# Kernel tuning notes

Measured on AMD Instinct MI355X. Metric: run time of the kernel, lower is better.

## Reference

```python
import jax, jax.numpy as jnp
import numpy as np

B, T, S, E, H, F = 4, 1024, 1024, 512, 8, 2048
D = E // H  # head_dim = 64
SCALE = D ** -0.5
EPS = 1e-5


def setup_inputs() -> dict:
    key = jax.random.key(0)
    ks = jax.random.split(key, 16)
    w = lambda k, shape: jax.random.normal(k, shape, jnp.float32) * 0.02
    inp = {
        'tgt': jax.random.normal(ks[0], (B, T, E), jnp.float32),
        'memory': jax.random.normal(ks[1], (B, S, E), jnp.float32),
    }
    for i, n in enumerate(['sWq', 'sWk', 'sWv', 'sWo', 'cWq', 'cWk', 'cWv', 'cWo']):
        inp[n] = w(ks[2 + i], (E, E))
    for n in ['sbq', 'sbk', 'sbv', 'sbo', 'cbq', 'cbk', 'cbv', 'cbo']:
        inp[n] = jnp.zeros((E,), jnp.float32)
    inp['fW1'] = w(ks[10], (E, F)); inp['fb1'] = jnp.zeros((F,), jnp.float32)
    inp['fW2'] = w(ks[11], (F, E)); inp['fb2'] = jnp.zeros((E,), jnp.float32)
    for n in ['g1', 'g2', 'g3']:
        inp[n] = jnp.ones((E,), jnp.float32)
    for n in ['be1', 'be2', 'be3']:
        inp[n] = jnp.zeros((E,), jnp.float32)
    return inp


def _ln(x, g, b):
    mu = jnp.mean(x, axis=-1, keepdims=True)
    var = jnp.mean(jnp.square(x - mu), axis=-1, keepdims=True)
    return (x - mu) * jax.lax.rsqrt(var + EPS) * g + b


def _mha(xq, xkv, Wq, bq, Wk, bk, Wv, bv, Wo, bo):
    # dense-equivalent of full N^2 edge-list attention (softmax over source nodes per target)
    Bq, Tq, _ = xq.shape
    Skv = xkv.shape[1]
    q = (xq @ Wq + bq).reshape(Bq, Tq, H, D)
    k = (xkv @ Wk + bk).reshape(Bq, Skv, H, D)
    v = (xkv @ Wv + bv).reshape(Bq, Skv, H, D)
    scores = jnp.einsum('bthd,bshd->bhts', q, k) * SCALE
    wts = jax.nn.softmax(scores, axis=-1)
    out = jnp.einsum('bhts,bshd->bthd', wts, v).reshape(Bq, Tq, E)
    return out @ Wo + bo


def reference(tgt, memory,
              sWq, sbq, sWk, sbk, sWv, sbv, sWo, sbo,
              cWq, cbq, cWk, cbk, cWv, cbv, cWo, cbo,
              fW1, fb1, fW2, fb2,
              g1, be1, g2, be2, g3, be3):
    # post-norm decoder layer: self-attn -> cross-attn -> FFN (dropout=0 eval)
    x = _ln(tgt + _mha(tgt, tgt, sWq, sbq, sWk, sbk, sWv, sbv, sWo, sbo), g1, be1)
    x = _ln(x + _mha(x, memory, cWq, cbq, cWk, cbk, cWv, cbv, cWo, cbo), g2, be2)
    ff = jax.nn.relu(x @ fW1 + fb1) @ fW2 + fb2
    x = _ln(x + ff, g3, be3)
    return x
```

## Files before the change

kernel.cpp:

```cpp
#include <hip/hip_runtime.h>

typedef unsigned short ushort_t;
typedef short short8 __attribute__((ext_vector_type(8)));
typedef float float4v __attribute__((ext_vector_type(4)));

__device__ __forceinline__ float bf2f(ushort_t u) {
    union { unsigned int i; float f; } x; x.i = ((unsigned int)u) << 16; return x.f;
}
__device__ __forceinline__ ushort_t f2bf(float f) {
    unsigned int u = __float_as_uint(f);
    unsigned int r = (u + 0x7FFFu + ((u >> 16) & 1u)) >> 16;
    return (ushort_t)r;
}
__device__ __forceinline__ void store_out(float* p, float v) { *p = v; }
__device__ __forceinline__ void store_out(ushort_t* p, float v) { *p = f2bf(v); }

__device__ __forceinline__ void gll16(const ushort_t* g, ushort_t* l) {
    __builtin_amdgcn_global_load_lds(
        (const __attribute__((address_space(1))) void*)g,
        (__attribute__((address_space(3))) void*)l, 16, 0, 0);
}

__global__ void detect_dtype(const ushort_t* __restrict__ tgt, int* __restrict__ flag) {
    __shared__ int red[256];
    const int tid = threadIdx.x;
    int p = 0;
    for (int i = tid; i < 512; i += 256) {
        ushort_t u = tgt[i];
        int e = (u >> 7) & 0xFF;
        if (u == 0 || (e >= 100 && e <= 140)) ++p;
    }
    red[tid] = p; __syncthreads();
    for (int off = 128; off > 0; off >>= 1) {
        if (tid < off) red[tid] += red[tid + off];
        __syncthreads();
    }
    if (tid == 0) flag[0] = (red[0] >= 480) ? 1 : 0;
}

__global__ __launch_bounds__(256) void prep_all(
    const void* sWq, const void* sWk, const void* sWv, const void* sWo,
    const void* cWq, const void* cWk, const void* cWv, const void* cWo,
    const void* fW1, const void* fW2,
    const void* tgt, const void* mem,
    const void* sbq, const void* sbk, const void* sbv, const void* sbo,
    const void* cbq, const void* cbk, const void* cbv, const void* cbo,
    const void* fb1, const void* fb2,
    ushort_t* __restrict__ wb, ushort_t* __restrict__ tb, ushort_t* __restrict__ mb,
    float* __restrict__ pb, const int* __restrict__ dflag)
{
    const bool f32 = (dflag[0] == 0);
    const int tid = threadIdx.x;
    const int z = blockIdx.z;

    if (z < 10) {
        const void* src; ushort_t* dst; int Kd, Nd;
        switch (z) {
            case 0: src = sWq; dst = wb + 0;       Kd = 512;  Nd = 512;  break;
            case 1: src = sWk; dst = wb + 262144;  Kd = 512;  Nd = 512;  break;
            case 2: src = sWv; dst = wb + 524288;  Kd = 512;  Nd = 512;  break;
            case 3: src = sWo; dst = wb + 786432;  Kd = 512;  Nd = 512;  break;
            case 4: src = cWq; dst = wb + 1048576; Kd = 512;  Nd = 512;  break;
            case 5: src = cWk; dst = wb + 1310720; Kd = 512;  Nd = 512;  break;
            case 6: src = cWv; dst = wb + 1572864; Kd = 512;  Nd = 512;  break;
            case 7: src = cWo; dst = wb + 1835008; Kd = 512;  Nd = 512;  break;
            case 8: src = fW1; dst = wb + 2097152; Kd = 512;  Nd = 2048; break;
            default:src = fW2; dst = wb + 3145728; Kd = 2048; Nd = 512;  break;
        }
        const int k0 = blockIdx.x * 64, n0 = blockIdx.y * 64;
        if (k0 >= Kd || n0 >= Nd) return;
        __shared__ ushort_t T[64][65];
#pragma unroll
        for (int i = 0; i < 16; ++i) {
            int j = i * 256 + tid;
            int r = j >> 6, c = j & 63;
            float v = f32 ? ((const float*)src)[(size_t)(k0 + r) * Nd + n0 + c]
                          : bf2f(((const ushort_t*)src)[(size_t)(k0 + r) * Nd + n0 + c]);
            T[r][c] = f2bf(v);
        }
        __syncthreads();
#pragma unroll
        for (int i = 0; i < 16; ++i) {
            int j = i * 256 + tid;
            int n = j >> 6, k = j & 63;
            dst[(size_t)(n0 + n) * Kd + k0 + k] = T[k][n];
        }
        return;
    }

    const int bid = blockIdx.x * 32 + blockIdx.y;
    if (z < 12) {
        const void* src = (z == 10) ? tgt : mem;
        ushort_t* dst = (z == 10) ? tb : mb;
        const int i = (bid * 256 + tid) * 8;
        if (f32) {
            float4 v0 = *(const float4*)((const float*)src + i);
            float4 v1 = *(const float4*)((const float*)src + i + 4);
            ushort_t o[8] = { f2bf(v0.x), f2bf(v0.y), f2bf(v0.z), f2bf(v0.w),
                              f2bf(v1.x), f2bf(v1.y), f2bf(v1.z), f2bf(v1.w) };
            *(uint4*)(dst + i) = *(const uint4*)o;
        } else {
            *(uint4*)(dst + i) = *(const uint4*)((const ushort_t*)src + i);
        }
        return;
    }

    {
        const int i = bid * 256 + tid;
        if (bid >= 26 || i >= 6656) return;
        const void* src; int off;
        if      (i < 512)  { src = sbq; off = i; }
        else if (i < 1024) { src = sbk; off = i - 512; }
        else if (i < 1536) { src = sbv; off = i - 1024; }
        else if (i < 2048) { src = sbo; off = i - 1536; }
        else if (i < 2560) { src = cbq; off = i - 2048; }
        else if (i < 3072) { src = cbk; off = i - 2560; }
        else if (i < 3584) { src = cbv; off = i - 3072; }
        else if (i < 4096) { src = cbo; off = i - 3584; }
        else if (i < 6144) { src = fb1; off = i - 4096; }
        else               { src = fb2; off = i - 6144; }
        pb[i] = f32 ? ((const float*)src)[off] : bf2f(((const ushort_t*)src)[off]);
    }
}

template<typename OutT, bool RELU, int BN>
__global__ __launch_bounds__(256) void gemm_tn(
    const ushort_t* __restrict__ A1, const ushort_t* __restrict__ A2,
    int ySplit, int lda,
    const ushort_t* __restrict__ Wt, int ldw,
    const float* __restrict__ bias,
    OutT* __restrict__ C, int ldc, int K)
{
    constexpr int MI = (BN == 128) ? 4 : 2;
    __shared__ ushort_t As[2][128][32];
    __shared__ ushort_t Bs[2][BN][32];
    const int tid = threadIdx.x;
    const int wave = tid >> 6, lane = tid & 63;
    const int quad = lane >> 4, l16 = lane & 15;
    const int m0 = blockIdx.x * 128, n0 = blockIdx.y * BN;
    const int wm = (BN == 128) ? (wave >> 1) * 64 : wave * 32;
    const int wn = (BN == 128) ? (wave & 1) * 64 : 0;
    const ushort_t* A = (((int)blockIdx.y) < ySplit) ? A1 : A2;

    float4v acc[MI][4];
#pragma unroll
    for (int mi = 0; mi < MI; ++mi)
#pragma unroll
        for (int ni = 0; ni < 4; ++ni) {
            acc[mi][ni][0] = 0.f; acc[mi][ni][1] = 0.f;
            acc[mi][ni][2] = 0.f; acc[mi][ni][3] = 0.f;
        }

    const int srow = lane >> 2;
    const int scc  = lane & 3;
    const int sg   = (scc - (lane >> 3)) & 3;
    const ushort_t* aptr0 = A  + (size_t)(m0 + wave * 16 + srow) * lda + sg * 8;
    const ushort_t* aptr1 = A  + (size_t)(m0 + 64 + wave * 16 + srow) * lda + sg * 8;
    const ushort_t* bptr0 = Wt + (size_t)(n0 + wave * 16 + srow) * ldw + sg * 8;
    const ushort_t* bptr1 = Wt + (size_t)(n0 + 64 + wave * 16 + srow) * ldw + sg * 8;

    gll16(aptr0, &As[0][wave * 16][0]);
    gll16(aptr1, &As[0][64 + wave * 16][0]);
    gll16(bptr0, &Bs[0][wave * 16][0]);
    if (BN == 128) gll16(bptr1, &Bs[0][64 + wave * 16][0]);

    const int ca = ((quad + (l16 >> 1)) & 3) * 8;
    int cur = 0;
    for (int k0 = 0; k0 < K; k0 += 32) {
        __syncthreads();
        if (k0 + 32 < K) {
            const int nb = cur ^ 1, ko = k0 + 32;
            gll16(aptr0 + ko, &As[nb][wave * 16][0]);
            gll16(aptr1 + ko, &As[nb][64 + wave * 16][0]);
            gll16(bptr0 + ko, &Bs[nb][wave * 16][0]);
            if (BN == 128) gll16(bptr1 + ko, &Bs[nb][64 + wave * 16][0]);
        }
        short8 af[MI], bfr[4];
#pragma unroll
        for (int mi = 0; mi < MI; ++mi)
            af[mi] = *(const short8*)(&As[cur][wm + mi * 16 + l16][ca]);
#pragma unroll
        for (int ni = 0; ni < 4; ++ni)
            bfr[ni] = *(const short8*)(&Bs[cur][wn + ni * 16 + l16][ca]);
#pragma unroll
        for (int mi = 0; mi < MI; ++mi)
#pragma unroll
            for (int ni = 0; ni < 4; ++ni)
                acc[mi][ni] = __builtin_amdgcn_mfma_f32_16x16x32_bf16(
                    af[mi], bfr[ni], acc[mi][ni], 0, 0, 0);
        cur ^= 1;
    }

#pragma unroll
    for (int ni = 0; ni < 4; ++ni) {
        const int col = n0 + wn + ni * 16 + l16;
        const float bv = bias[col];
#pragma unroll
        for (int mi = 0; mi < MI; ++mi)
#pragma unroll
            for (int r = 0; r < 4; ++r) {
                const int row = m0 + wm + mi * 16 + quad * 4 + r;
                float v = acc[mi][ni][r] + bv;
                if (RELU) v = fmaxf(v, 0.f);
                store_out(&C[(size_t)row * ldc + col], v);
            }
    }
}

__global__ __launch_bounds__(512) void attn_mfma(ushort_t* __restrict__ QKV)
{
    const int S = 1536;
    __shared__ ushort_t PsA[64][72];
    __shared__ ushort_t PsB[64][72];
    __shared__ ushort_t Ks[2][64][72];
    __shared__ ushort_t Vt[2][64][72];

    const int tid  = threadIdx.x;
    const int w    = tid >> 6;
    const int g    = w >> 2;
    const int wq   = w & 3;
    const int lane = tid & 63;
    const int quad = lane >> 4, l16 = lane & 15;
    const int ht   = tid & 255;
    const int qt = blockIdx.x, bh = blockIdx.y;
    const int b = bh >> 3, h = bh & 7;
    const size_t rowQ = (size_t)b * 1024 + qt * 64;
    const size_t kv0  = (size_t)b * 1024;

    const int kr = ht >> 2, kc = (ht & 3) * 16;
    const int sp = ht >> 3, dc = (ht & 7) * 8;
    const int vr0 = sp * 2;
    const int vrg = vr0 >> 3, vrof = vr0 & 7;

    {
        const int r = tid >> 3, c = (tid & 7) * 8;
        *(uint4*)(&PsA[r][c]) = *(const uint4*)(QKV + (rowQ + r) * S + h * 64 + c);
    }
    __syncthreads();
    short8 qf[2];
    qf[0] = *(const short8*)(&PsA[wq * 16 + l16][quad * 8]);
    qf[1] = *(const short8*)(&PsA[wq * 16 + l16][32 + quad * 8]);
    ushort_t (* __restrict__ Ps)[72] = g ? PsB : PsA;

    const float CEXP = 0.125f * 1.44269504f;
    const float MREF = 16.0f * CEXP;
    float lsum[4];
    float4v oacc[4];
#pragma unroll
    for (int r = 0; r < 4; ++r) lsum[r] = 0.f;
#pragma unroll
    for (int n = 0; n < 4; ++n) { oacc[n][0]=0.f; oacc[n][1]=0.f; oacc[n][2]=0.f; oacc[n][3]=0.f; }

    uint4 kA, kB, vA, vB;
    {
        const size_t sr = kv0 + g * 64;
        const ushort_t* ksrc = QKV + (sr + kr) * S + 512 + h * 64 + kc;
        kA = *(const uint4*)(ksrc);
        kB = *(const uint4*)(ksrc + 8);
        const ushort_t* vsrc = QKV + (sr + vr0) * S + 1024 + h * 64 + dc;
        vA = *(const uint4*)(vsrc);
        vB = *(const uint4*)(vsrc + S);
    }

    for (int it = 0; it < 8; ++it) {
        __syncthreads();
        *(uint4*)(&Ks[g][kr][kc])     = kA;
        *(uint4*)(&Ks[g][kr][kc + 8]) = kB;
        {
            const ushort_t* ae = (const ushort_t*)&vA;
            const ushort_t* be = (const ushort_t*)&vB;
#pragma unroll
            for (int j = 0; j < 8; ++j) {
                const int d = dc + j;
                const int cc = (vrg ^ (d >> 4)) & 7;
                *(unsigned int*)(&Vt[g][d][cc * 8 + vrof]) =
                    (unsigned int)ae[j] | ((unsigned int)be[j] << 16);
            }
        }
        __syncthreads();
        if (it < 7) {
            const size_t sr = kv0 + (it + 1) * 128 + g * 64;
            const ushort_t* ksrc = QKV + (sr + kr) * S + 512 + h * 64 + kc;
            kA = *(const uint4*)(ksrc);
            kB = *(const uint4*)(ksrc + 8);
            const ushort_t* vsrc = QKV + (sr + vr0) * S + 1024 + h * 64 + dc;
            vA = *(const uint4*)(vsrc);
            vB = *(const uint4*)(vsrc + S);
        }

        float4v sc[4];
#pragma unroll
        for (int sb = 0; sb < 4; ++sb) {
            float4v z; z[0]=0.f; z[1]=0.f; z[2]=0.f; z[3]=0.f;
            short8 kf0 = *(const short8*)(&Ks[g][sb * 16 + l16][quad * 8]);
            short8 kf1 = *(const short8*)(&Ks[g][sb * 16 + l16][32 + quad * 8]);
            z = __builtin_amdgcn_mfma_f32_16x16x32_bf16(qf[0], kf0, z, 0, 0, 0);
            z = __builtin_amdgcn_mfma_f32_16x16x32_bf16(qf[1], kf1, z, 0, 0, 0);
            sc[sb] = z;
        }

#pragma unroll
        for (int sb = 0; sb < 4; ++sb)
#pragma unroll
            for (int r = 0; r < 4; ++r) {
                float p = exp2f(fmaf(sc[sb][r], CEXP, -MREF));
                lsum[r] += p;
                Ps[wq * 16 + quad * 4 + r][sb * 16 + l16] = f2bf(p);
            }

        short8 pf[2];
        pf[0] = *(const short8*)(&Ps[wq * 16 + l16][quad * 8]);
        pf[1] = *(const short8*)(&Ps[wq * 16 + l16][32 + quad * 8]);
#pragma unroll
        for (int n = 0; n < 4; ++n) {
#pragma unroll
            for (int kc2 = 0; kc2 < 2; ++kc2) {
                const int cc = ((kc2 * 4 + quad) ^ n) & 7;
                short8 vf = *(const short8*)(&Vt[g][n * 16 + l16][cc * 8]);
                oacc[n] = __builtin_amdgcn_mfma_f32_16x16x32_bf16(pf[kc2], vf, oacc[n], 0, 0, 0);
            }
        }
    }

#pragma unroll
    for (int msk = 1; msk < 16; msk <<= 1)
#pragma unroll
        for (int r = 0; r < 4; ++r) lsum[r] += __shfl_xor(lsum[r], msk);

    float* exch = (float*)&Ks[0][0][0];
    float* exl  = (float*)&Vt[0][0][0];
    __syncthreads();
    if (g == 1) {
#pragma unroll
        for (int n = 0; n < 4; ++n)
#pragma unroll
            for (int r = 0; r < 4; ++r)
                exch[((wq * 4 + n) * 4 + r) * 64 + lane] = oacc[n][r];
        if (l16 == 0)
#pragma unroll
            for (int r = 0; r < 4; ++r) exl[wq * 16 + quad * 4 + r] = lsum[r];
    }
    __syncthreads();
    if (g == 0) {
#pragma unroll
        for (int r = 0; r < 4; ++r) lsum[r] += exl[wq * 16 + quad * 4 + r];
        float inv[4];
#pragma unroll
        for (int r = 0; r < 4; ++r) inv[r] = 1.f / lsum[r];
#pragma unroll
        for (int n = 0; n < 4; ++n)
#pragma unroll
            for (int r = 0; r < 4; ++r) {
                float o = oacc[n][r] + exch[((wq * 4 + n) * 4 + r) * 64 + lane];
                const size_t row = rowQ + wq * 16 + quad * 4 + r;
                QKV[row * S + h * 64 + n * 16 + l16] = f2bf(o * inv[r]);
            }
    }
}

template<bool RES_EXT, bool DELTA_F32, bool OUT_FLAG>
__global__ __launch_bounds__(256) void ln_kernel(
    const void* __restrict__ res, const void* __restrict__ delta,
    const void* __restrict__ g, const void* __restrict__ be,
    void* __restrict__ out, const int* __restrict__ dflag)
{
    const int E = 512;
    const bool extf32 = (dflag[0] == 0);
    const int row = blockIdx.x, tid = threadIdx.x;
    const int wave = tid >> 6, lane = tid & 63;
    const size_t base = (size_t)row * E;
    const int i0 = tid, i1 = tid + 256;

    float r0, r1;
    if (RES_EXT && extf32) {
        r0 = ((const float*)res)[base + i0];
        r1 = ((const float*)res)[base + i1];
    } else {
        r0 = bf2f(((const ushort_t*)res)[base + i0]);
        r1 = bf2f(((const ushort_t*)res)[base + i1]);
    }
    float d0v, d1v;
    if (DELTA_F32) {
        d0v = ((const float*)delta)[base + i0];
        d1v = ((const float*)delta)[base + i1];
    } else {
        d0v = bf2f(((const ushort_t*)delta)[base + i0]);
        d1v = bf2f(((const ushort_t*)delta)[base + i1]);
    }
    float x0 = r0 + d0v, x1 = r1 + d1v;

    __shared__ float red8[8];
    float s = x0 + x1;
#pragma unroll
    for (int m = 1; m < 64; m <<= 1) s += __shfl_xor(s, m);
    if (lane == 0) red8[wave] = s;
    __syncthreads();
    float mean = (red8[0] + red8[1] + red8[2] + red8[3]) * (1.0f / 512.0f);
    float dd0 = x0 - mean, dd1 = x1 - mean;
    float v = dd0 * dd0 + dd1 * dd1;
#pragma unroll
    for (int m = 1; m < 64; m <<= 1) v += __shfl_xor(v, m);
    if (lane == 0) red8[4 + wave] = v;
    __syncthreads();
    float rstd = rsqrtf((red8[4] + red8[5] + red8[6] + red8[7]) * (1.0f / 512.0f) + 1e-5f);

    float g0, g1v, b0, b1;
    if (extf32) {
        g0 = ((const float*)g)[i0];  g1v = ((const float*)g)[i1];
        b0 = ((const float*)be)[i0]; b1  = ((const float*)be)[i1];
    } else {
        g0 = bf2f(((const ushort_t*)g)[i0]);  g1v = bf2f(((const ushort_t*)g)[i1]);
        b0 = bf2f(((const ushort_t*)be)[i0]); b1  = bf2f(((const ushort_t*)be)[i1]);
    }
    float y0 = dd0 * rstd * g0 + b0;
    float y1 = dd1 * rstd * g1v + b1;
    if (OUT_FLAG && extf32) {
        ((float*)out)[base + i0] = y0; ((float*)out)[base + i1] = y1;
    } else {
        ((ushort_t*)out)[base + i0] = f2bf(y0);
        ((ushort_t*)out)[base + i1] = f2bf(y1);
    }
}


extern "C" void kernel_launch(void* const* d_in, const int* in_sizes, int n_in,
                              void* d_out, int out_size, void* d_ws, size_t ws_size,
                              hipStream_t stream) {
    const void* tgt = d_in[0];
    const void* mem = d_in[1];
    const void* sWq = d_in[2];  const void* sWk = d_in[3];
    const void* sWv = d_in[4];  const void* sWo = d_in[5];
    const void* cWq = d_in[6];  const void* cWk = d_in[7];
    const void* cWv = d_in[8];  const void* cWo = d_in[9];
    const void* sbq = d_in[10]; const void* sbk = d_in[11];
    const void* sbv = d_in[12]; const void* sbo = d_in[13];
    const void* cbq = d_in[14]; const void* cbk = d_in[15];
    const void* cbv = d_in[16]; const void* cbo = d_in[17];
    const void* fW1 = d_in[18]; const void* fb1 = d_in[19];
    const void* fW2 = d_in[20]; const void* fb2 = d_in[21];
    const void* g1  = d_in[22]; const void* g2  = d_in[23];
    const void* g3  = d_in[24];
    const void* be1 = d_in[25]; const void* be2 = d_in[26];
    const void* be3 = d_in[27];

    char* ws = (char*)d_ws;
    const size_t MB = 1048576;
    ushort_t* qkv = (ushort_t*)(ws + 0 * MB);
    ushort_t* hb  = (ushort_t*)(ws + 0 * MB);
    ushort_t* po  = (ushort_t*)(ws + 12 * MB);
    ushort_t* xb  = (ushort_t*)(ws + 16 * MB);
    ushort_t* tb  = (ushort_t*)(ws + 20 * MB);
    ushort_t* mb  = (ushort_t*)(ws + 24 * MB);
    float*    of  = (float*)   (ws + 20 * MB);
    ushort_t* wb  = (ushort_t*)(ws + 28 * MB);
    float*    pb  = (float*)   (ws + 36 * MB);
    int*   dflag  = (int*)     (ws + 36 * MB + 262144);

    const ushort_t* sWqkv_t = wb + 0;
    const ushort_t* sWo_t   = wb + 786432;
    const ushort_t* cWqkv_t = wb + 1048576;
    const ushort_t* cWo_t   = wb + 1835008;
    const ushort_t* fW1_t   = wb + 2097152;
    const ushort_t* fW2_t   = wb + 3145728;

    dim3 blk(256);

    detect_dtype<<<dim3(1), blk, 0, stream>>>((const ushort_t*)tgt, dflag);
    prep_all<<<dim3(32, 32, 13), blk, 0, stream>>>(
        sWq, sWk, sWv, sWo, cWq, cWk, cWv, cWo, fW1, fW2,
        tgt, mem, sbq, sbk, sbv, sbo, cbq, cbk, cbv, cbo, fb1, fb2,
        wb, tb, mb, pb, dflag);

    dim3 gattn(16, 32);
    dim3 blk512(512);

    gemm_tn<ushort_t, false, 128><<<dim3(32, 12), blk, 0, stream>>>(tb, tb, 0, 512, sWqkv_t, 512, pb + 0, qkv, 1536, 512);
    attn_mfma<<<gattn, blk512, 0, stream>>>(qkv);
    gemm_tn<ushort_t, false, 64><<<dim3(32, 8), blk, 0, stream>>>(qkv, qkv, 0, 1536, sWo_t, 512, pb + 1536, po, 512, 512);
    ln_kernel<true, false, false><<<dim3(4096), blk, 0, stream>>>(tgt, po, g1, be1, xb, dflag);

    gemm_tn<ushort_t, false, 128><<<dim3(32, 12), blk, 0, stream>>>(xb, mb, 4, 512, cWqkv_t, 512, pb + 2048, qkv, 1536, 512);
    attn_mfma<<<gattn, blk512, 0, stream>>>(qkv);
    gemm_tn<ushort_t, false, 64><<<dim3(32, 8), blk, 0, stream>>>(qkv, qkv, 0, 1536, cWo_t, 512, pb + 3584, po, 512, 512);
    ln_kernel<false, false, false><<<dim3(4096), blk, 0, stream>>>(xb, po, g2, be2, xb, dflag);

    gemm_tn<ushort_t, true, 128><<<dim3(32, 16), blk, 0, stream>>>(xb, xb, 0, 512, fW1_t, 512, pb + 4096, hb, 2048, 512);
    gemm_tn<float, false, 64><<<dim3(32, 8), blk, 0, stream>>>(hb, hb, 0, 2048, fW2_t, 2048, pb + 6144, of, 512, 2048);
    ln_kernel<false, true, true><<<dim3(4096), blk, 0, stream>>>(xb, of, g3, be3, d_out, dflag);
}
```

Before: 299.3 us.

## Split K across wave groups in narrow GEMMs and fold dtype detection into prep

The N=512 output GEMMs (attention out-projections and FFN down-projection) move to a 512-thread kernel. Two groups of four waves each handle half of K, and their partial sums are reduced through LDS before the bias is added and the result stored. This gives more waves per block on a grid of only 256 blocks, so latency is hidden better. The separate detect_dtype launch is removed: every prep block recomputes the detection itself, and one block writes the flag for the later LN kernels. The cost is redundant detection work in every prep block, plus extra LDS and syncs for the split-K reduction.

```diff
diff --git a/kernel.cpp b/kernel.cpp
--- a/kernel.cpp
+++ b/kernel.cpp
@@ -19,23 +19,6 @@
     __builtin_amdgcn_global_load_lds(
         (const __attribute__((address_space(1))) void*)g,
         (__attribute__((address_space(3))) void*)l, 16, 0, 0);
-}
-
-__global__ void detect_dtype(const ushort_t* __restrict__ tgt, int* __restrict__ flag) {
-    __shared__ int red[256];
-    const int tid = threadIdx.x;
-    int p = 0;
-    for (int i = tid; i < 512; i += 256) {
-        ushort_t u = tgt[i];
-        int e = (u >> 7) & 0xFF;
-        if (u == 0 || (e >= 100 && e <= 140)) ++p;
-    }
-    red[tid] = p; __syncthreads();
-    for (int off = 128; off > 0; off >>= 1) {
-        if (tid < off) red[tid] += red[tid + off];
-        __syncthreads();
-    }
-    if (tid == 0) flag[0] = (red[0] >= 480) ? 1 : 0;
 }
 
 __global__ __launch_bounds__(256) void prep_all(
@@ -47,11 +30,26 @@
     const void* cbq, const void* cbk, const void* cbv, const void* cbo,
     const void* fb1, const void* fb2,
     ushort_t* __restrict__ wb, ushort_t* __restrict__ tb, ushort_t* __restrict__ mb,
-    float* __restrict__ pb, const int* __restrict__ dflag)
+    float* __restrict__ pb, int* __restrict__ dflag)
 {
-    const bool f32 = (dflag[0] == 0);
     const int tid = threadIdx.x;
     const int z = blockIdx.z;
+
+    __shared__ int red[256];
+    {
+        int p = 0;
+        for (int i = tid; i < 512; i += 256) {
+            ushort_t u = ((const ushort_t*)tgt)[i];
+            int e = (u >> 7) & 0xFF;
+            if (u == 0 || (e >= 100 && e <= 140)) ++p;
+        }
+        red[tid] = p; __syncthreads();
+        for (int off = 128; off > 0; off >>= 1) {
+            if (tid < off) red[tid] += red[tid + off];
+            __syncthreads();
+        }
+    }
+    const bool f32 = (red[0] < 480);
 
     if (z < 10) {
         const void* src; ushort_t* dst; int Kd, Nd;
@@ -106,6 +104,7 @@
     }
 
     {
+        if (bid == 26) { if (tid == 0) dflag[0] = f32 ? 0 : 1; return; }
         const int i = bid * 256 + tid;
         if (bid >= 26 || i >= 6656) return;
         const void* src; int off;
@@ -123,7 +122,7 @@
     }
 }
 
-template<typename OutT, bool RELU, int BN>
+template<typename OutT, bool RELU>
 __global__ __launch_bounds__(256) void gemm_tn(
     const ushort_t* __restrict__ A1, const ushort_t* __restrict__ A2,
     int ySplit, int lda,
@@ -131,20 +130,18 @@
     const float* __restrict__ bias,
     OutT* __restrict__ C, int ldc, int K)
 {
-    constexpr int MI = (BN == 128) ? 4 : 2;
     __shared__ ushort_t As[2][128][32];
-    __shared__ ushort_t Bs[2][BN][32];
+    __shared__ ushort_t Bs[2][128][32];
     const int tid = threadIdx.x;
     const int wave = tid >> 6, lane = tid & 63;
     const int quad = lane >> 4, l16 = lane & 15;
-    const int m0 = blockIdx.x * 128, n0 = blockIdx.y * BN;
-    const int wm = (BN == 128) ? (wave >> 1) * 64 : wave * 32;
-    const int wn = (BN == 128) ? (wave & 1) * 64 : 0;
+    const int m0 = blockIdx.x * 128, n0 = blockIdx.y * 128;
+    const int wm = (wave >> 1) * 64, wn = (wave & 1) * 64;
     const ushort_t* A = (((int)blockIdx.y) < ySplit) ? A1 : A2;
 
-    float4v acc[MI][4];
-#pragma unroll
-    for (int mi = 0; mi < MI; ++mi)
+    float4v acc[4][4];
+#pragma unroll
+    for (int mi = 0; mi < 4; ++mi)
 #pragma unroll
         for (int ni = 0; ni < 4; ++ni) {
             acc[mi][ni][0] = 0.f; acc[mi][ni][1] = 0.f;
@@ -162,7 +159,7 @@
     gll16(aptr0, &As[0][wave * 16][0]);
     gll16(aptr1, &As[0][64 + wave * 16][0]);
     gll16(bptr0, &Bs[0][wave * 16][0]);
-    if (BN == 128) gll16(bptr1, &Bs[0][64 + wave * 16][0]);
+    gll16(bptr1, &Bs[0][64 + wave * 16][0]);
 
     const int ca = ((quad + (l16 >> 1)) & 3) * 8;
     int cur = 0;
@@ -173,17 +170,17 @@
             gll16(aptr0 + ko, &As[nb][wave * 16][0]);
             gll16(aptr1 + ko, &As[nb][64 + wave * 16][0]);
             gll16(bptr0 + ko, &Bs[nb][wave * 16][0]);
-            if (BN == 128) gll16(bptr1 + ko, &Bs[nb][64 + wave * 16][0]);
-        }
-        short8 af[MI], bfr[4];
-#pragma unroll
-        for (int mi = 0; mi < MI; ++mi)
+            gll16(bptr1 + ko, &Bs[nb][64 + wave * 16][0]);
+        }
+        short8 af[4], bfr[4];
+#pragma unroll
+        for (int mi = 0; mi < 4; ++mi)
             af[mi] = *(const short8*)(&As[cur][wm + mi * 16 + l16][ca]);
 #pragma unroll
         for (int ni = 0; ni < 4; ++ni)
             bfr[ni] = *(const short8*)(&Bs[cur][wn + ni * 16 + l16][ca]);
 #pragma unroll
-        for (int mi = 0; mi < MI; ++mi)
+        for (int mi = 0; mi < 4; ++mi)
 #pragma unroll
             for (int ni = 0; ni < 4; ++ni)
                 acc[mi][ni] = __builtin_amdgcn_mfma_f32_16x16x32_bf16(
@@ -196,7 +193,7 @@
         const int col = n0 + wn + ni * 16 + l16;
         const float bv = bias[col];
 #pragma unroll
-        for (int mi = 0; mi < MI; ++mi)
+        for (int mi = 0; mi < 4; ++mi)
 #pragma unroll
             for (int r = 0; r < 4; ++r) {
                 const int row = m0 + wm + mi * 16 + quad * 4 + r;
@@ -204,6 +201,100 @@
                 if (RELU) v = fmaxf(v, 0.f);
                 store_out(&C[(size_t)row * ldc + col], v);
             }
+    }
+}
+
+template<typename OutT, bool RELU>
+__global__ __launch_bounds__(512) void gemm_tn_sk(
+    const ushort_t* __restrict__ A, int lda,
+    const ushort_t* __restrict__ Wt, int ldw,
+    const float* __restrict__ bias,
+    OutT* __restrict__ C, int ldc, int K)
+{
+    __shared__ ushort_t As[2][2][128][32];
+    __shared__ ushort_t Bs[2][2][64][32];
+    const int tid = threadIdx.x;
+    const int wave = tid >> 6, lane = tid & 63;
+    const int g = wave >> 2, wq = wave & 3;
+    const int quad = lane >> 4, l16 = lane & 15;
+    const int m0 = blockIdx.x * 128, n0 = blockIdx.y * 64;
+    const int wm = wq * 32;
+    const int Kh = K >> 1, kbase = g * Kh;
+
+    float4v acc[2][4];
+#pragma unroll
+    for (int mi = 0; mi < 2; ++mi)
+#pragma unroll
+        for (int ni = 0; ni < 4; ++ni) {
+            acc[mi][ni][0] = 0.f; acc[mi][ni][1] = 0.f;
+            acc[mi][ni][2] = 0.f; acc[mi][ni][3] = 0.f;
+        }
+
+    const int srow = lane >> 2;
+    const int scc  = lane & 3;
+    const int sg   = (scc - (lane >> 3)) & 3;
+    const ushort_t* aptr0 = A  + (size_t)(m0 + wq * 16 + srow) * lda + kbase + sg * 8;
+    const ushort_t* aptr1 = A  + (size_t)(m0 + 64 + wq * 16 + srow) * lda + kbase + sg * 8;
+    const ushort_t* bptr0 = Wt + (size_t)(n0 + wq * 16 + srow) * ldw + kbase + sg * 8;
+
+    gll16(aptr0, &As[g][0][wq * 16][0]);
+    gll16(aptr1, &As[g][0][64 + wq * 16][0]);
+    gll16(bptr0, &Bs[g][0][wq * 16][0]);
+
+    const int ca = ((quad + (l16 >> 1)) & 3) * 8;
+    int cur = 0;
+    for (int k0 = 0; k0 < Kh; k0 += 32) {
+        __syncthreads();
+        if (k0 + 32 < Kh) {
+            const int nb = cur ^ 1, ko = k0 + 32;
+            gll16(aptr0 + ko, &As[g][nb][wq * 16][0]);
+            gll16(aptr1 + ko, &As[g][nb][64 + wq * 16][0]);
+            gll16(bptr0 + ko, &Bs[g][nb][wq * 16][0]);
+        }
+        short8 af[2], bfr[4];
+#pragma unroll
+        for (int mi = 0; mi < 2; ++mi)
+            af[mi] = *(const short8*)(&As[g][cur][wm + mi * 16 + l16][ca]);
+#pragma unroll
+        for (int ni = 0; ni < 4; ++ni)
+            bfr[ni] = *(const short8*)(&Bs[g][cur][ni * 16 + l16][ca]);
+#pragma unroll
+        for (int mi = 0; mi < 2; ++mi)
+#pragma unroll
+            for (int ni = 0; ni < 4; ++ni)
+                acc[mi][ni] = __builtin_amdgcn_mfma_f32_16x16x32_bf16(
+                    af[mi], bfr[ni], acc[mi][ni], 0, 0, 0);
+        cur ^= 1;
+    }
+
+    __syncthreads();
+    float* ex = (float*)&As[0][0][0][0];
+    const int ht = tid & 255;
+    if (g == 1) {
+#pragma unroll
+        for (int mi = 0; mi < 2; ++mi)
+#pragma unroll
+            for (int ni = 0; ni < 4; ++ni)
+#pragma unroll
+                for (int r = 0; r < 4; ++r)
+                    ex[ht * 32 + mi * 16 + ni * 4 + r] = acc[mi][ni][r];
+    }
+    __syncthreads();
+    if (g == 0) {
+#pragma unroll
+        for (int ni = 0; ni < 4; ++ni) {
+            const int col = n0 + ni * 16 + l16;
+            const float bv = bias[col];
+#pragma unroll
+            for (int mi = 0; mi < 2; ++mi)
+#pragma unroll
+                for (int r = 0; r < 4; ++r) {
+                    const int row = m0 + wm + mi * 16 + quad * 4 + r;
+                    float v = acc[mi][ni][r] + ex[ht * 32 + mi * 16 + ni * 4 + r] + bv;
+                    if (RELU) v = fmaxf(v, 0.f);
+                    store_out(&C[(size_t)row * ldc + col], v);
+                }
+        }
     }
 }
 
@@ -463,28 +554,25 @@
     const ushort_t* fW1_t   = wb + 2097152;
     const ushort_t* fW2_t   = wb + 3145728;
 
-    dim3 blk(256);
-
-    detect_dtype<<<dim3(1), blk, 0, stream>>>((const ushort_t*)tgt, dflag);
+    dim3 blk(256), blk512(512);
+    dim3 gattn(16, 32);
+
     prep_all<<<dim3(32, 32, 13), blk, 0, stream>>>(
         sWq, sWk, sWv, sWo, cWq, cWk, cWv, cWo, fW1, fW2,
         tgt, mem, sbq, sbk, sbv, sbo, cbq, cbk, cbv, cbo, fb1, fb2,
         wb, tb, mb, pb, dflag);
 
-    dim3 gattn(16, 32);
-    dim3 blk512(512);
-
-    gemm_tn<ushort_t, false, 128><<<dim3(32, 12), blk, 0, stream>>>(tb, tb, 0, 512, sWqkv_t, 512, pb + 0, qkv, 1536, 512);
+    gemm_tn<ushort_t, false><<<dim3(32, 12), blk, 0, stream>>>(tb, tb, 0, 512, sWqkv_t, 512, pb + 0, qkv, 1536, 512);
     attn_mfma<<<gattn, blk512, 0, stream>>>(qkv);
-    gemm_tn<ushort_t, false, 64><<<dim3(32, 8), blk, 0, stream>>>(qkv, qkv, 0, 1536, sWo_t, 512, pb + 1536, po, 512, 512);
+    gemm_tn_sk<ushort_t, false><<<dim3(32, 8), blk512, 0, stream>>>(qkv, 1536, sWo_t, 512, pb + 1536, po, 512, 512);
     ln_kernel<true, false, false><<<dim3(4096), blk, 0, stream>>>(tgt, po, g1, be1, xb, dflag);
 
-    gemm_tn<ushort_t, false, 128><<<dim3(32, 12), blk, 0, stream>>>(xb, mb, 4, 512, cWqkv_t, 512, pb + 2048, qkv, 1536, 512);
+    gemm_tn<ushort_t, false><<<dim3(32, 12), blk, 0, stream>>>(xb, mb, 4, 512, cWqkv_t, 512, pb + 2048, qkv, 1536, 512);
     attn_mfma<<<gattn, blk512, 0, stream>>>(qkv);
-    gemm_tn<ushort_t, false, 64><<<dim3(32, 8), blk, 0, stream>>>(qkv, qkv, 0, 1536, cWo_t, 512, pb + 3584, po, 512, 512);
+    gemm_tn_sk<ushort_t, false><<<dim3(32, 8), blk512, 0, stream>>>(qkv, 1536, cWo_t, 512, pb + 3584, po, 512, 512);
     ln_kernel<false, false, false><<<dim3(4096), blk, 0, stream>>>(xb, po, g2, be2, xb, dflag);
 
-    gemm_tn<ushort_t, true, 128><<<dim3(32, 16), blk, 0, stream>>>(xb, xb, 0, 512, fW1_t, 512, pb + 4096, hb, 2048, 512);
-    gemm_tn<float, false, 64><<<dim3(32, 8), blk, 0, stream>>>(hb, hb, 0, 2048, fW2_t, 2048, pb + 6144, of, 512, 2048);
+    gemm_tn<ushort_t, true><<<dim3(32, 16), blk, 0, stream>>>(xb, xb, 0, 512, fW1_t, 512, pb + 4096, hb, 2048, 512);
+    gemm_tn_sk<float, false><<<dim3(32, 8), blk512, 0, stream>>>(hb, 2048, fW2_t, 2048, pb + 6144, of, 512, 2048);
     ln_kernel<false, true, true><<<dim3(4096), blk, 0, stream>>>(xb, of, g3, be3, d_out, dflag);
 }
```

Result: no change. 303.1 us (+1.2%).
